# Optimization experiments

Measured on AMD Instinct MI355X. Metric: run time of the kernel, lower is better.

Reference implementation:

```python
import jax, jax.numpy as jnp
import numpy as np

INPUT_DIM = 1024
OUTPUT_DIM = 1024
NUM_HEADS = 16  # NOTE: torch .split(num_heads) => chunk SIZE = num_heads
N_CHUNKS = OUTPUT_DIM // NUM_HEADS  # 64 effective heads of dim 16
NEG_INF = -1e9


def setup_inputs() -> dict:
    key = jax.random.key(0)
    k1, k2, k3, k4 = jax.random.split(key, 4)
    B, S = 32, 256
    x = jax.random.normal(k1, (B, S, INPUT_DIM), dtype=jnp.float32)
    mask = jnp.ones((B, S), dtype=jnp.float32)
    # xavier-uniform-ish linear weights, torch layout [out, in]
    lim = float(np.sqrt(6.0 / (INPUT_DIM + OUTPUT_DIM)))
    Wq = jax.random.uniform(k2, (OUTPUT_DIM, INPUT_DIM), jnp.float32, -lim, lim)
    Wk = jax.random.uniform(k3, (OUTPUT_DIM, INPUT_DIM), jnp.float32, -lim, lim)
    Wv = jax.random.uniform(k4, (OUTPUT_DIM, INPUT_DIM), jnp.float32, -lim, lim)
    return {"batch_sequence": x, "sequence_mask": mask, "Wq": Wq, "Wk": Wk, "Wv": Wv}


def _split_heads(m):
    # [B,S,D] -> chunks of size NUM_HEADS stacked in dim 0: [C,B,S,H]
    B, S, D = m.shape
    return jnp.transpose(m.reshape(B, S, N_CHUNKS, NUM_HEADS), (2, 0, 1, 3))


def reference(batch_sequence, sequence_mask, Wq, Wk, Wv):
    q = _split_heads(batch_sequence @ Wq.T)  # [C,B,S,H]
    k = _split_heads(batch_sequence @ Wk.T)
    v = _split_heads(batch_sequence @ Wv.T)
    logits = jnp.einsum("cbqh,cbkh->cbqk", q, k) / jnp.sqrt(
        jnp.asarray(OUTPUT_DIM, batch_sequence.dtype)
    )
    mask2d = sequence_mask[:, :, None] * sequence_mask[:, None, :]  # [B,S,S]
    logits = jnp.where(mask2d[None] > 0, logits, NEG_INF)
    w = jax.nn.softmax(logits, axis=-1)
    out = jnp.einsum("cbqk,cbkh->cbqh", w, v)  # [C,B,S,H]
    B, S = batch_sequence.shape[:2]
    return jnp.transpose(out, (1, 2, 0, 3)).reshape(B, S, OUTPUT_DIM)
```

## Files before the change

kernel.cpp:

```cpp
#include <hip/hip_runtime.h>


typedef unsigned short u16;
typedef unsigned int u32;
typedef __attribute__((ext_vector_type(8))) short short8;
typedef __attribute__((ext_vector_type(4))) short short4v;
typedef __attribute__((ext_vector_type(4))) float floatx4;

#if __has_builtin(__builtin_amdgcn_mfma_f32_16x16x16bf16_1k)
#define MFMA16(A, B, C) __builtin_amdgcn_mfma_f32_16x16x16bf16_1k(A, B, C, 0, 0, 0)
#elif __has_builtin(__builtin_amdgcn_mfma_f32_16x16x16_bf16)
#define MFMA16(A, B, C) __builtin_amdgcn_mfma_f32_16x16x16_bf16(A, B, C, 0, 0, 0)
#else
__device__ __forceinline__ floatx4 mfma16_asm(short4v a, short4v b, floatx4 c) {
  floatx4 d;
  asm volatile("v_mfma_f32_16x16x16_bf16 %0, %1, %2, %3"
               : "=v"(d) : "v"(a), "v"(b), "v"(c));
  return d;
}
#define MFMA16(A, B, C) mfma16_asm(A, B, C)
#endif

#if __has_builtin(__builtin_amdgcn_exp2f)
#define EXP2(x) __builtin_amdgcn_exp2f(x)
#else
#define EXP2(x) __expf((x) * 0.6931471805599453f)
#endif

#define QSCALE 0.045084220f

__device__ __forceinline__ u16 f2bf(float f) {
  union { float f; u32 u; } x; x.f = f;
  u32 r = x.u + 0x7fffu + ((x.u >> 16) & 1u);
  return (u16)(r >> 16);
}
__device__ __forceinline__ float bf2f(u16 u) {
  union { u32 u; float f; } x; x.u = ((u32)u) << 16;
  return x.f;
}

__device__ __forceinline__ void gload16(const void* g, void* l) {
  typedef __attribute__((address_space(1))) const unsigned int gq;
  typedef __attribute__((address_space(3))) unsigned int lq;
  __builtin_amdgcn_global_load_lds((gq*)(size_t)g, (lq*)(size_t)l, 16, 0, 0);
}

#define GK 1024
#define QKS 20
#define VTS 264

__global__ __launch_bounds__(256) void cast_all(const float* __restrict__ x,
                                                const float* __restrict__ wq,
                                                const float* __restrict__ wk,
                                                const float* __restrict__ wv,
                                                u16* __restrict__ XB,
                                                u16* __restrict__ WB) {
  int bid = blockIdx.x;
  const float* src; u16* dst; int off;
  if (bid < 8192)       { src = x;  dst = XB;                 off = bid; }
  else if (bid < 9216)  { src = wq; dst = WB;                 off = bid - 8192; }
  else if (bid < 10240) { src = wk; dst = WB + 1024 * 1024;   off = bid - 9216; }
  else                  { src = wv; dst = WB + 2 * 1024 * 1024; off = bid - 10240; }
  int i = (off * 256 + threadIdx.x) * 4;
  float4 v = *(const float4*)(src + i);
  u32 lo = (u32)f2bf(v.x) | ((u32)f2bf(v.y) << 16);
  u32 hi = (u32)f2bf(v.z) | ((u32)f2bf(v.w) << 16);
  uint2 o; o.x = lo; o.y = hi;
  *(uint2*)(dst + i) = o;
}

template <bool MASKED>
__device__ __forceinline__ void attn_loop(const u16* __restrict__ Ks,
                                          const u16* __restrict__ Vt,
                                          const short4v* bq, const float* mqv,
                                          const float* m_s,
                                          floatx4* oacc, floatx4* lacc,
                                          int col, int quad) {
  const short4v ones = {(short)0x3F80, (short)0x3F80, (short)0x3F80, (short)0x3F80};
#pragma unroll 4
  for (int kt = 0; kt < 16; kt++) {
    const int kb = kt * 16;
    short4v ak = *(const short4v*)(Ks + (kb + col) * QKS + quad * 4);
    short4v av = *(const short4v*)(Vt + col * VTS + kb + quad * 4);
    float mk[4];
    if (MASKED) {
#pragma unroll
      for (int i = 0; i < 4; i++) mk[i] = m_s[kb + quad * 4 + i];
    }
#pragma unroll
    for (int qt = 0; qt < 4; qt++) {
      floatx4 z = {0.f, 0.f, 0.f, 0.f};
      floatx4 st = MFMA16(ak, bq[qt], z);
      float e[4];
#pragma unroll
      for (int i = 0; i < 4; i++) {
        e[i] = EXP2(st[i]);
        if (MASKED) e[i] = (mqv[qt] * mk[i] > 0.f) ? e[i] : 0.f;
      }
      union { u32 u[2]; short4v s; } pk;
      pk.u[0] = __builtin_amdgcn_perm(__float_as_uint(e[1]), __float_as_uint(e[0]), 0x07060302u);
      pk.u[1] = __builtin_amdgcn_perm(__float_as_uint(e[3]), __float_as_uint(e[2]), 0x07060302u);
      lacc[qt] = MFMA16(ones, pk.s, lacc[qt]);
      oacc[qt] = MFMA16(av, pk.s, oacc[qt]);
    }
  }
}

__global__ __launch_bounds__(256) void fused_qkv_attn(const u16* __restrict__ XB,
                                                      const u16* __restrict__ WB,
                                                      const float* __restrict__ mask,
                                                      float* __restrict__ out) {
  __shared__ u16 smem[19456];
  __shared__ float m_s[256];

  const int bid = blockIdx.x;
  const int b = bid & 31;
  const int c = bid >> 5;
  const int t = threadIdx.x;
  const int wave = t >> 6;
  const int lane = t & 63;
  const int col = lane & 15;
  const int quad = lane >> 4;

  u16* Xs = smem;
  u16* Ws = smem + 16384;

  float mv = mask[b * 256 + t];
  m_s[t] = mv;
  const int allones = __syncthreads_and(mv > 0.f);

  const int r_loc = lane >> 3;
  const int xb = (lane & 7) ^ r_loc;

  floatx4 acc[4][3] = {};

  const size_t xrow = ((size_t)b * 256 + wave * 64 + r_loc) * GK + xb * 8;
  const int wg0 = wave * 2;
  int wrow0 = 0, wrow1 = 0;
  if (wave < 3) {
    int wr0 = wg0 * 8 + r_loc, wr1 = wr0 + 8;
    wrow0 = (wr0 >> 4) * 1024 + c * 16 + (wr0 & 15);
    wrow1 = (wr1 >> 4) * 1024 + c * 16 + (wr1 & 15);
  }

  for (int k0 = 0; k0 < GK; k0 += 64) {
    __syncthreads();
#pragma unroll
    for (int i = 0; i < 8; i++)
      gload16(XB + xrow + (size_t)i * 8 * GK + k0, Xs + (wave * 64 + i * 8) * 64);
    if (wave < 3) {
      gload16(WB + (size_t)wrow0 * GK + k0 + xb * 8, Ws + (wg0 * 8) * 64);
      gload16(WB + (size_t)wrow1 * GK + k0 + xb * 8, Ws + (wg0 * 8 + 8) * 64);
    }
    __syncthreads();
#pragma unroll
    for (int kk = 0; kk < 2; kk++) {
      const int pos = ((kk * 4 + quad) ^ (lane & 7)) * 8;
      short8 af[4], bf[3];
#pragma unroll
      for (int mt = 0; mt < 4; mt++)
        af[mt] = *(const short8*)(Xs + (wave * 64 + mt * 16 + col) * 64 + pos);
#pragma unroll
      for (int nt = 0; nt < 3; nt++)
        bf[nt] = *(const short8*)(Ws + (nt * 16 + col) * 64 + pos);
#pragma unroll
      for (int mt = 0; mt < 4; mt++)
#pragma unroll
        for (int nt = 0; nt < 3; nt++)
          acc[mt][nt] = __builtin_amdgcn_mfma_f32_16x16x32_bf16(af[mt], bf[nt], acc[mt][nt], 0, 0, 0);
    }
  }

  __syncthreads();
  u16* Qs = smem;
  u16* Ks = smem + 5120;
  u16* Vt = smem + 10240;
  float* l_s = (float*)(smem + 14464);

#pragma unroll
  for (int mt = 0; mt < 4; mt++) {
    const int row = wave * 64 + mt * 16 + quad * 4;
#pragma unroll
    for (int r = 0; r < 4; r++) {
      Qs[(row + r) * QKS + col] = f2bf(acc[mt][0][r] * QSCALE);
      Ks[(row + r) * QKS + col] = f2bf(acc[mt][1][r]);
      Vt[col * VTS + row + r] = f2bf(acc[mt][2][r]);
    }
  }
  __syncthreads();

  const int q0 = wave * 64;

  short4v bq[4];
#pragma unroll
  for (int qt = 0; qt < 4; qt++)
    bq[qt] = *(const short4v*)(Qs + (q0 + qt * 16 + col) * QKS + quad * 4);

  float mqv[4];
#pragma unroll
  for (int qt = 0; qt < 4; qt++) mqv[qt] = m_s[q0 + qt * 16 + col];

  floatx4 oacc[4] = {};
  floatx4 lacc[4] = {};

  if (allones)
    attn_loop<false>(Ks, Vt, bq, mqv, m_s, oacc, lacc, col, quad);
  else
    attn_loop<true>(Ks, Vt, bq, mqv, m_s, oacc, lacc, col, quad);

  __syncthreads();
  float* ot = (float*)smem;

#pragma unroll
  for (int qt = 0; qt < 4; qt++) {
    if (quad == 0) l_s[q0 + qt * 16 + col] = lacc[qt][0];
#pragma unroll
    for (int r = 0; r < 4; r++)
      ot[(quad * 4 + r) * 257 + q0 + qt * 16 + col] = oacc[qt][r];
  }
  __syncthreads();

  float l = l_s[t];
  float* op = out + ((size_t)b * 256 + t) * 1024 + c * 16;
  float o[16];
  if (allones || l > 0.f) {
    float inv = 1.0f / l;
#pragma unroll
    for (int h = 0; h < 16; h++) o[h] = ot[h * 257 + t] * inv;
  } else {
#pragma unroll
    for (int h = 0; h < 16; h++) o[h] = 0.f;
    for (int k = 0; k < 256; k++)
#pragma unroll
      for (int h = 0; h < 16; h++) o[h] += bf2f(Vt[h * VTS + k]);
#pragma unroll
    for (int h = 0; h < 16; h++) o[h] *= (1.0f / 256.0f);
  }
#pragma unroll
  for (int g = 0; g < 4; g++) {
    float4 r;
    r.x = o[g * 4 + 0]; r.y = o[g * 4 + 1]; r.z = o[g * 4 + 2]; r.w = o[g * 4 + 3];
    *(float4*)(op + g * 4) = r;
  }
}

extern "C" void kernel_launch(void* const* d_in, const int* in_sizes, int n_in,
                              void* d_out, int out_size, void* d_ws, size_t ws_size,
                              hipStream_t stream) {
  const float* x    = (const float*)d_in[0];
  const float* mask = (const float*)d_in[1];
  const float* Wq   = (const float*)d_in[2];
  const float* Wk   = (const float*)d_in[3];
  const float* Wv   = (const float*)d_in[4];
  float* out = (float*)d_out;

  u16* XB = (u16*)d_ws;
  u16* WB = XB + (size_t)8192 * 1024;

  cast_all<<<11264, 256, 0, stream>>>(x, Wq, Wk, Wv, XB, WB);
  fused_qkv_attn<<<2048, 256, 0, stream>>>(XB, WB, mask, out);
}
```

Before: 176.3 us.

## Double-buffer the QKV projection K-loop with async LDS prefetch

```diff
diff --git a/kernel.cpp b/kernel.cpp
--- a/kernel.cpp
+++ b/kernel.cpp
@@ -110,7 +110,7 @@
                                                       const u16* __restrict__ WB,
                                                       const float* __restrict__ mask,
                                                       float* __restrict__ out) {
-  __shared__ u16 smem[19456];
+  __shared__ __align__(16) u16 smem[19456];
   __shared__ float m_s[256];
 
   const int bid = blockIdx.x;
@@ -122,53 +122,76 @@
   const int col = lane & 15;
   const int quad = lane >> 4;
 
-  u16* Xs = smem;
-  u16* Ws = smem + 16384;
+  u16* const Xs0 = smem;
+  u16* const Xs1 = smem + 8192;
+  u16* const Ws0 = smem + 16384;
+  u16* const Ws1 = smem + 17920;
 
   float mv = mask[b * 256 + t];
   m_s[t] = mv;
   const int allones = __syncthreads_and(mv > 0.f);
 
-  const int r_loc = lane >> 3;
-  const int xb = (lane & 7) ^ r_loc;
+  const int rl = lane >> 2;
+  const int ch = lane & 3;
+  const int sch = ch ^ (rl & 3);
+  const size_t xsrc = ((size_t)b * 256 + wave * 64 + rl) * GK + sch * 8;
+  const int xdst = wave * 2048;
+  size_t wsrc = 0;
+  if (wave < 3)
+    wsrc = ((size_t)wave * 1024 + c * 16 + rl) * GK + sch * 8;
+  const int wdst = wave * 512;
 
   floatx4 acc[4][3] = {};
 
-  const size_t xrow = ((size_t)b * 256 + wave * 64 + r_loc) * GK + xb * 8;
-  const int wg0 = wave * 2;
-  int wrow0 = 0, wrow1 = 0;
-  if (wave < 3) {
-    int wr0 = wg0 * 8 + r_loc, wr1 = wr0 + 8;
-    wrow0 = (wr0 >> 4) * 1024 + c * 16 + (wr0 & 15);
-    wrow1 = (wr1 >> 4) * 1024 + c * 16 + (wr1 & 15);
-  }
-
-  for (int k0 = 0; k0 < GK; k0 += 64) {
-    __syncthreads();
-#pragma unroll
-    for (int i = 0; i < 8; i++)
-      gload16(XB + xrow + (size_t)i * 8 * GK + k0, Xs + (wave * 64 + i * 8) * 64);
-    if (wave < 3) {
-      gload16(WB + (size_t)wrow0 * GK + k0 + xb * 8, Ws + (wg0 * 8) * 64);
-      gload16(WB + (size_t)wrow1 * GK + k0 + xb * 8, Ws + (wg0 * 8 + 8) * 64);
-    }
-    __syncthreads();
-#pragma unroll
-    for (int kk = 0; kk < 2; kk++) {
-      const int pos = ((kk * 4 + quad) ^ (lane & 7)) * 8;
-      short8 af[4], bf[3];
-#pragma unroll
-      for (int mt = 0; mt < 4; mt++)
-        af[mt] = *(const short8*)(Xs + (wave * 64 + mt * 16 + col) * 64 + pos);
+  const int ropos = (quad ^ (col & 3)) * 8;
+  const int arow = (wave * 64 + col) * 32 + ropos;
+
+#pragma unroll
+  for (int g = 0; g < 4; g++)
+    gload16(XB + xsrc + (size_t)g * 16 * GK, Xs0 + xdst + g * 512);
+  if (wave < 3) gload16(WB + wsrc, Ws0 + wdst);
+
+#pragma unroll 2
+  for (int tt = 0; tt < 32; tt++) {
+    u16* const Xc = (tt & 1) ? Xs1 : Xs0;
+    u16* const Wc = (tt & 1) ? Ws1 : Ws0;
+    u16* const Xn = (tt & 1) ? Xs0 : Xs1;
+    u16* const Wn = (tt & 1) ? Ws0 : Ws1;
+
+    if (tt < 31) {
+      const int k0n = (tt + 1) * 32;
+#pragma unroll
+      for (int g = 0; g < 4; g++)
+        gload16(XB + xsrc + (size_t)g * 16 * GK + k0n, Xn + xdst + g * 512);
+      if (wave < 3) {
+        gload16(WB + wsrc + k0n, Wn + wdst);
+        asm volatile("s_waitcnt vmcnt(5)" ::: "memory");
+      } else {
+        asm volatile("s_waitcnt vmcnt(4)" ::: "memory");
+      }
+    } else {
+      asm volatile("s_waitcnt vmcnt(0)" ::: "memory");
+    }
+    __builtin_amdgcn_sched_barrier(0);
+    __builtin_amdgcn_s_barrier();
+    __builtin_amdgcn_sched_barrier(0);
+
+    short8 af[4], bf[3];
+#pragma unroll
+    for (int mt = 0; mt < 4; mt++)
+      af[mt] = *(const short8*)(Xc + arow + mt * 512);
+#pragma unroll
+    for (int nt = 0; nt < 3; nt++)
+      bf[nt] = *(const short8*)(Wc + (nt * 16 + col) * 32 + ropos);
+#pragma unroll
+    for (int mt = 0; mt < 4; mt++)
 #pragma unroll
       for (int nt = 0; nt < 3; nt++)
-        bf[nt] = *(const short8*)(Ws + (nt * 16 + col) * 64 + pos);
-#pragma unroll
-      for (int mt = 0; mt < 4; mt++)
-#pragma unroll
-        for (int nt = 0; nt < 3; nt++)
-          acc[mt][nt] = __builtin_amdgcn_mfma_f32_16x16x32_bf16(af[mt], bf[nt], acc[mt][nt], 0, 0, 0);
-    }
+        acc[mt][nt] = __builtin_amdgcn_mfma_f32_16x16x32_bf16(af[mt], bf[nt], acc[mt][nt], 0, 0, 0);
+
+    asm volatile("s_waitcnt lgkmcnt(0)" ::: "memory");
+    __builtin_amdgcn_sched_barrier(0);
+    __builtin_amdgcn_s_barrier();
   }
 
   __syncthreads();
```

New measurement: 196.7 us. 1.12x slower.

## Process two head chunks per block with 512 threads to reuse X tiles

Applied to the files above, without the earlier changes.

```diff
diff --git a/kernel.cpp b/kernel.cpp
--- a/kernel.cpp
+++ b/kernel.cpp
@@ -70,12 +70,12 @@
 }
 
 template <bool MASKED>
-__device__ __forceinline__ void attn_loop(const u16* __restrict__ Ks,
-                                          const u16* __restrict__ Vt,
-                                          const short4v* bq, const float* mqv,
-                                          const float* m_s,
-                                          floatx4* oacc, floatx4* lacc,
-                                          int col, int quad) {
+__device__ __forceinline__ void attn_loop2(const u16* __restrict__ Ks,
+                                           const u16* __restrict__ Vt,
+                                           const short4v* bq, const float* mqv,
+                                           const float* m_s,
+                                           floatx4* oacc, floatx4* lacc,
+                                           int col, int quad) {
   const short4v ones = {(short)0x3F80, (short)0x3F80, (short)0x3F80, (short)0x3F80};
 #pragma unroll 4
   for (int kt = 0; kt < 16; kt++) {
@@ -88,7 +88,7 @@
       for (int i = 0; i < 4; i++) mk[i] = m_s[kb + quad * 4 + i];
     }
 #pragma unroll
-    for (int qt = 0; qt < 4; qt++) {
+    for (int qt = 0; qt < 2; qt++) {
       floatx4 z = {0.f, 0.f, 0.f, 0.f};
       floatx4 st = MFMA16(ak, bq[qt], z);
       float e[4];
@@ -106,141 +106,146 @@
   }
 }
 
-__global__ __launch_bounds__(256) void fused_qkv_attn(const u16* __restrict__ XB,
-                                                      const u16* __restrict__ WB,
-                                                      const float* __restrict__ mask,
-                                                      float* __restrict__ out) {
-  __shared__ u16 smem[19456];
+__global__ __launch_bounds__(512, 4) void fused_qkv_attn(const u16* __restrict__ XB,
+                                                         const u16* __restrict__ WB,
+                                                         const float* __restrict__ mask,
+                                                         float* __restrict__ out) {
+  __shared__ __align__(16) u16 smem[22528];
   __shared__ float m_s[256];
 
   const int bid = blockIdx.x;
   const int b = bid & 31;
-  const int c = bid >> 5;
+  const int c0 = (bid >> 5) * 2;
   const int t = threadIdx.x;
   const int wave = t >> 6;
   const int lane = t & 63;
   const int col = lane & 15;
   const int quad = lane >> 4;
 
-  u16* Xs = smem;
-  u16* Ws = smem + 16384;
-
-  float mv = mask[b * 256 + t];
-  m_s[t] = mv;
+  u16* const Xs = smem;
+  u16* const Ws = smem + 16384;
+
+  float mv = (t < 256) ? mask[b * 256 + t] : 1.0f;
+  if (t < 256) m_s[t] = mv;
   const int allones = __syncthreads_and(mv > 0.f);
 
   const int r_loc = lane >> 3;
-  const int xb = (lane & 7) ^ r_loc;
-
-  floatx4 acc[4][3] = {};
-
-  const size_t xrow = ((size_t)b * 256 + wave * 64 + r_loc) * GK + xb * 8;
-  const int wg0 = wave * 2;
-  int wrow0 = 0, wrow1 = 0;
-  if (wave < 3) {
-    int wr0 = wg0 * 8 + r_loc, wr1 = wr0 + 8;
-    wrow0 = (wr0 >> 4) * 1024 + c * 16 + (wr0 & 15);
-    wrow1 = (wr1 >> 4) * 1024 + c * 16 + (wr1 & 15);
-  }
+  const int sch = (lane & 7) ^ r_loc;
+
+  const size_t xsrc = ((size_t)b * 256 + wave * 32 + r_loc) * GK + sch * 8;
+  const int xdst = wave * 2048;
+
+  const int gA = wave;
+  const int ntA = gA >> 1;
+  const size_t wsrcA =
+      ((size_t)((ntA % 3) * 1024 + (c0 + ntA / 3) * 16 + (gA & 1) * 8 + r_loc)) * GK + sch * 8;
+  size_t wsrcB = 0;
+  const int gB = 8 + wave;
+  if (wave < 4) {
+    const int ntB = gB >> 1;
+    wsrcB = ((size_t)((ntB % 3) * 1024 + (c0 + ntB / 3) * 16 + (gB & 1) * 8 + r_loc)) * GK + sch * 8;
+  }
+
+  floatx4 acc[2][6] = {};
 
   for (int k0 = 0; k0 < GK; k0 += 64) {
     __syncthreads();
 #pragma unroll
-    for (int i = 0; i < 8; i++)
-      gload16(XB + xrow + (size_t)i * 8 * GK + k0, Xs + (wave * 64 + i * 8) * 64);
-    if (wave < 3) {
-      gload16(WB + (size_t)wrow0 * GK + k0 + xb * 8, Ws + (wg0 * 8) * 64);
-      gload16(WB + (size_t)wrow1 * GK + k0 + xb * 8, Ws + (wg0 * 8 + 8) * 64);
-    }
+    for (int g = 0; g < 4; g++)
+      gload16(XB + xsrc + (size_t)g * 8 * GK + k0, Xs + xdst + g * 512);
+    gload16(WB + wsrcA + k0, Ws + gA * 512);
+    if (wave < 4) gload16(WB + wsrcB + k0, Ws + gB * 512);
     __syncthreads();
 #pragma unroll
     for (int kk = 0; kk < 2; kk++) {
-      const int pos = ((kk * 4 + quad) ^ (lane & 7)) * 8;
-      short8 af[4], bf[3];
-#pragma unroll
-      for (int mt = 0; mt < 4; mt++)
-        af[mt] = *(const short8*)(Xs + (wave * 64 + mt * 16 + col) * 64 + pos);
-#pragma unroll
-      for (int nt = 0; nt < 3; nt++)
+      const int pos = ((kk * 4 + quad) ^ (col & 7)) * 8;
+      short8 af[2], bf[6];
+#pragma unroll
+      for (int mt = 0; mt < 2; mt++)
+        af[mt] = *(const short8*)(Xs + (wave * 32 + mt * 16 + col) * 64 + pos);
+#pragma unroll
+      for (int nt = 0; nt < 6; nt++)
         bf[nt] = *(const short8*)(Ws + (nt * 16 + col) * 64 + pos);
 #pragma unroll
-      for (int mt = 0; mt < 4; mt++)
-#pragma unroll
-        for (int nt = 0; nt < 3; nt++)
+      for (int mt = 0; mt < 2; mt++)
+#pragma unroll
+        for (int nt = 0; nt < 6; nt++)
           acc[mt][nt] = __builtin_amdgcn_mfma_f32_16x16x32_bf16(af[mt], bf[nt], acc[mt][nt], 0, 0, 0);
     }
   }
 
-  __syncthreads();
-  u16* Qs = smem;
-  u16* Ks = smem + 5120;
-  u16* Vt = smem + 10240;
-  float* l_s = (float*)(smem + 14464);
-
-#pragma unroll
-  for (int mt = 0; mt < 4; mt++) {
-    const int row = wave * 64 + mt * 16 + quad * 4;
-#pragma unroll
-    for (int r = 0; r < 4; r++) {
-      Qs[(row + r) * QKS + col] = f2bf(acc[mt][0][r] * QSCALE);
-      Ks[(row + r) * QKS + col] = f2bf(acc[mt][1][r]);
-      Vt[col * VTS + row + r] = f2bf(acc[mt][2][r]);
-    }
-  }
-  __syncthreads();
-
-  const int q0 = wave * 64;
-
-  short4v bq[4];
-#pragma unroll
-  for (int qt = 0; qt < 4; qt++)
-    bq[qt] = *(const short4v*)(Qs + (q0 + qt * 16 + col) * QKS + quad * 4);
-
-  float mqv[4];
-#pragma unroll
-  for (int qt = 0; qt < 4; qt++) mqv[qt] = m_s[q0 + qt * 16 + col];
-
-  floatx4 oacc[4] = {};
-  floatx4 lacc[4] = {};
-
-  if (allones)
-    attn_loop<false>(Ks, Vt, bq, mqv, m_s, oacc, lacc, col, quad);
-  else
-    attn_loop<true>(Ks, Vt, bq, mqv, m_s, oacc, lacc, col, quad);
-
-  __syncthreads();
-  float* ot = (float*)smem;
-
-#pragma unroll
-  for (int qt = 0; qt < 4; qt++) {
-    if (quad == 0) l_s[q0 + qt * 16 + col] = lacc[qt][0];
-#pragma unroll
-    for (int r = 0; r < 4; r++)
-      ot[(quad * 4 + r) * 257 + q0 + qt * 16 + col] = oacc[qt][r];
-  }
-  __syncthreads();
-
-  float l = l_s[t];
-  float* op = out + ((size_t)b * 256 + t) * 1024 + c * 16;
-  float o[16];
-  if (allones || l > 0.f) {
-    float inv = 1.0f / l;
-#pragma unroll
-    for (int h = 0; h < 16; h++) o[h] = ot[h * 257 + t] * inv;
-  } else {
-#pragma unroll
-    for (int h = 0; h < 16; h++) o[h] = 0.f;
-    for (int k = 0; k < 256; k++)
-#pragma unroll
-      for (int h = 0; h < 16; h++) o[h] += bf2f(Vt[h * VTS + k]);
-#pragma unroll
-    for (int h = 0; h < 16; h++) o[h] *= (1.0f / 256.0f);
-  }
-#pragma unroll
-  for (int g = 0; g < 4; g++) {
-    float4 r;
-    r.x = o[g * 4 + 0]; r.y = o[g * 4 + 1]; r.z = o[g * 4 + 2]; r.w = o[g * 4 + 3];
-    *(float4*)(op + g * 4) = r;
+  u16* const Qs = smem;
+  u16* const Ks = smem + 5120;
+  u16* const Vt = smem + 10240;
+  float* const l_s = (float*)(smem + 14464);
+  float* const ot = (float*)smem;
+
+#pragma unroll
+  for (int h = 0; h < 2; h++) {
+    __syncthreads();
+
+#pragma unroll
+    for (int mt = 0; mt < 2; mt++) {
+      const int row = wave * 32 + mt * 16 + quad * 4;
+#pragma unroll
+      for (int r = 0; r < 4; r++) {
+        Qs[(row + r) * QKS + col] = f2bf(acc[mt][3 * h + 0][r] * QSCALE);
+        Ks[(row + r) * QKS + col] = f2bf(acc[mt][3 * h + 1][r]);
+        Vt[col * VTS + row + r] = f2bf(acc[mt][3 * h + 2][r]);
+      }
+    }
+    __syncthreads();
+
+    const int q0 = wave * 32;
+    short4v bq[2];
+    float mqv[2];
+#pragma unroll
+    for (int qt = 0; qt < 2; qt++) {
+      bq[qt] = *(const short4v*)(Qs + (q0 + qt * 16 + col) * QKS + quad * 4);
+      mqv[qt] = m_s[q0 + qt * 16 + col];
+    }
+
+    floatx4 oacc[2] = {};
+    floatx4 lacc[2] = {};
+    if (allones)
+      attn_loop2<false>(Ks, Vt, bq, mqv, m_s, oacc, lacc, col, quad);
+    else
+      attn_loop2<true>(Ks, Vt, bq, mqv, m_s, oacc, lacc, col, quad);
+
+    __syncthreads();
+#pragma unroll
+    for (int qt = 0; qt < 2; qt++) {
+      if (quad == 0) l_s[q0 + qt * 16 + col] = lacc[qt][0];
+#pragma unroll
+      for (int r = 0; r < 4; r++)
+        ot[(quad * 4 + r) * 257 + q0 + qt * 16 + col] = oacc[qt][r];
+    }
+    __syncthreads();
+
+    const int row = t >> 1;
+    const int hb = (t & 1) * 8;
+    float l = l_s[row];
+    float* op = out + ((size_t)b * 256 + row) * 1024 + (c0 + h) * 16 + hb;
+    float o[8];
+    if (allones || l > 0.f) {
+      float inv = 1.0f / l;
+#pragma unroll
+      for (int j = 0; j < 8; j++) o[j] = ot[(hb + j) * 257 + row] * inv;
+    } else {
+#pragma unroll
+      for (int j = 0; j < 8; j++) o[j] = 0.f;
+      for (int k = 0; k < 256; k++)
+#pragma unroll
+        for (int j = 0; j < 8; j++) o[j] += bf2f(Vt[(hb + j) * VTS + k]);
+#pragma unroll
+      for (int j = 0; j < 8; j++) o[j] *= (1.0f / 256.0f);
+    }
+#pragma unroll
+    for (int g = 0; g < 2; g++) {
+      float4 r;
+      r.x = o[g * 4 + 0]; r.y = o[g * 4 + 1]; r.z = o[g * 4 + 2]; r.w = o[g * 4 + 3];
+      *(float4*)(op + g * 4) = r;
+    }
   }
 }
 
@@ -258,5 +263,5 @@
   u16* WB = XB + (size_t)8192 * 1024;
 
   cast_all<<<11264, 256, 0, stream>>>(x, Wq, Wk, Wv, XB, WB);
-  fused_qkv_attn<<<2048, 256, 0, stream>>>(XB, WB, mask, out);
-}
+  fused_qkv_attn<<<1024, 512, 0, stream>>>(XB, WB, mask, out);
+}
```

Result: faster. 165.2 us (-6.3%).
